# Kernel optimization log

Measured on AMD Instinct MI355X. Metric: run time of the kernel, lower is better.

Reference implementation:

```python
import jax, jax.numpy as jnp
import numpy as np
from jax import lax

B, H, W = 128, 128, 128
CHANS = [3, 32, 64, 128]   # convolution_structure
F, FH, FW = 128, 16, 16    # n_features, feature map size after 3 maxpools
P = FH * FW                # flatten_feature_size = 256
E, OUT = 32, 53            # expert_output_len, output_len


def _conv(x, w, b):
    # NCHW conv, 3x3, SAME padding, stride 1
    y = lax.conv_general_dilated(x, w, (1, 1), 'SAME',
                                 dimension_numbers=('NCHW', 'OIHW', 'NCHW'))
    return y + b[None, :, None, None]


def _maxpool2(x):
    return lax.reduce_window(x, -jnp.inf, lax.max,
                             (1, 1, 2, 2), (1, 1, 2, 2), 'VALID')


def setup_inputs() -> dict:
    key = jax.random.key(0)
    ks = jax.random.split(key, 16)

    def n(k, shape, fan_in):
        return jax.random.normal(k, shape, jnp.float32) / np.float32(np.sqrt(fan_in))

    inp = {'x': jax.random.normal(ks[0], (B, CHANS[0], H, W), jnp.float32)}
    for i in range(3):
        cin, cout = CHANS[i], CHANS[i + 1]
        inp[f'cw{i + 1}'] = n(ks[1 + i], (cout, cin, 3, 3), cin * 9)
        inp[f'cb{i + 1}'] = jnp.zeros((cout,), jnp.float32)
    inp['Wa'] = n(ks[4], (F, P), P)
    inp['ba'] = jnp.zeros((F,), jnp.float32)
    # per-expert MLP 256 -> 256 -> 128 -> 32 (128 experts, batched)
    inp['ew1'] = n(ks[5], (F, 256, 256), 256)
    inp['eb1'] = jnp.zeros((F, 256), jnp.float32)
    inp['ew2'] = n(ks[6], (F, 256, 128), 256)
    inp['eb2'] = jnp.zeros((F, 128), jnp.float32)
    inp['ew3'] = n(ks[7], (F, 128, E), 128)
    inp['eb3'] = jnp.zeros((F, E), jnp.float32)
    inp['fw'] = n(ks[8], (F * E, OUT), F * E)
    inp['fb'] = jnp.zeros((OUT,), jnp.float32)
    return inp


def reference(x, cw1, cb1, cw2, cb2, cw3, cb3, Wa, ba,
              ew1, eb1, ew2, eb2, ew3, eb3, fw, fb):
    # CNNBlock: (conv3x3 + ReLU + maxpool2) x 3  -> [B, F, 16, 16]
    h = x
    for w, b in ((cw1, cb1), (cw2, cb2), (cw3, cb3)):
        h = _maxpool2(jax.nn.relu(_conv(h, w, b)))
    feat = h.reshape(h.shape[0], F, P)                        # [B, F, 256]

    # AttentionBlock: per-feature scalar gate (attention_value = 1)
    att = jax.nn.sigmoid(jnp.einsum('bfp,fp->bf', feat, Wa) + ba)[:, :, None]

    # Experts: 128 independent gated MLPs, batched as grouped GEMMs
    z = feat * att                                            # input gating
    z = jax.nn.relu(jnp.einsum('bfp,fpq->bfq', z, ew1) + eb1)
    z = jax.nn.relu(jnp.einsum('bfp,fpq->bfq', z, ew2) + eb2)
    z = jnp.einsum('bfp,fpq->bfq', z, ew3) + eb3              # [B, F, 32]

    # outer ReLU over stacked expert outputs, flatten, final dense (att=1)
    z = jax.nn.relu(z).reshape(z.shape[0], -1)                # [B, 4096]
    return z @ fw + fb                                        # [B, 53]
```

## Files before the change

### kernel.cpp

```cpp
#include <hip/hip_runtime.h>
#include <hip/hip_bf16.h>
#include <math.h>

#define NF 128
#define NP 256

typedef __attribute__((ext_vector_type(8))) short bf16x8;
typedef __attribute__((ext_vector_type(4))) short bf16x4;
typedef __attribute__((ext_vector_type(4))) float f32x4;

#define GLOBAL_AS __attribute__((address_space(1)))
#define LDS_AS __attribute__((address_space(3)))

__global__ void __launch_bounds__(256) wpack_k(const float* __restrict__ w,
                                               __hip_bfloat16* __restrict__ wp,
                                               int COUT, int CIN)
{
    int i = blockIdx.x * 256 + threadIdx.x;
    int total = 9 * COUT * CIN;
    if (i >= total) return;
    int o  = i / (COUT * CIN);
    int r  = i - o * (COUT * CIN);
    int co = r / CIN, ci = r - co * CIN;
    wp[i] = __float2bfloat16(w[(size_t)(co * CIN + ci) * 9 + o]);
}

__global__ void __launch_bounds__(256) wpack1_k(const float* __restrict__ w,
                                                __hip_bfloat16* __restrict__ wp1)
{
    int i = blockIdx.x * 256 + threadIdx.x;
    if (i >= 2048) return;
    int s = i >> 10, co = (i >> 5) & 31, k = i & 31;
    int o = s * 8 + (k >> 2), ch = k & 3;
    float v = 0.f;
    if (o < 9 && ch < 3) v = w[(size_t)(co * 3 + ch) * 9 + o];
    wp1[i] = __float2bfloat16(v);
}

__global__ void __launch_bounds__(256) x2cl_k(const float* __restrict__ x,
                                              __hip_bfloat16* __restrict__ xb)
{
    int i = blockIdx.x * 256 + threadIdx.x;
    int b = i >> 14, rem = i & 16383;
    size_t base = ((size_t)b * 3) << 14;
    float v0 = x[base + rem];
    float v1 = x[base + 16384 + rem];
    float v2 = x[base + 32768 + rem];
    unsigned short hv[4];
    __hip_bfloat16 h0 = __float2bfloat16(v0);
    __hip_bfloat16 h1 = __float2bfloat16(v1);
    __hip_bfloat16 h2 = __float2bfloat16(v2);
    __builtin_memcpy(&hv[0], &h0, 2);
    __builtin_memcpy(&hv[1], &h1, 2);
    __builtin_memcpy(&hv[2], &h2, 2);
    hv[3] = 0;
    *(int2*)(xb + (size_t)i * 4) = *(const int2*)hv;
}

__global__ void __launch_bounds__(256) tpack_k(const float* __restrict__ in,
                                               __hip_bfloat16* __restrict__ out,
                                               int P, int Q, int qtiles)
{
    const int f  = blockIdx.y;
    const int pt = blockIdx.x / qtiles, qt = blockIdx.x - pt * qtiles;
    __shared__ float t[32][33];
    const float* src = in + (size_t)f * P * Q;
    __hip_bfloat16* dst = out + (size_t)f * P * Q;
    const int rr = threadIdx.x >> 5, c = threadIdx.x & 31;
    #pragma unroll
    for (int i = 0; i < 4; ++i)
        t[rr + i * 8][c] = src[(size_t)(pt * 32 + rr + i * 8) * Q + qt * 32 + c];
    __syncthreads();
    #pragma unroll
    for (int i = 0; i < 4; ++i)
        dst[(size_t)(qt * 32 + rr + i * 8) * P + pt * 32 + c] =
            __float2bfloat16(t[c][rr + i * 8]);
}

__global__ void __launch_bounds__(256) fwt_k(const float* __restrict__ fw, float* __restrict__ fwt)
{
    int i = blockIdx.x * 256 + threadIdx.x;
    if (i >= 53 * 4096) return;
    int o = i >> 12, k = i & 4095;
    fwt[i] = fw[(size_t)k * 53 + o];
}

__global__ void __launch_bounds__(256, 2) conv1_mfma(
    const __hip_bfloat16* __restrict__ xb,
    const __hip_bfloat16* __restrict__ wp1,
    const float* __restrict__ bias,
    __hip_bfloat16* __restrict__ out)
{
    __shared__ char lds[14 * 130 * 8];
    const int rb  = blockIdx.x * 8;
    const int b   = blockIdx.z;
    const int tid = threadIdx.x;

    #pragma unroll
    for (int t = 0; t < 8; ++t) {
        int u = tid + t * 256;
        if (u < 14 * 130) {
            int px = u % 130, row = u / 130;
            int gy = rb + row - 1, gx = px - 1;
            int2 v = make_int2(0, 0);
            if (gy >= 0 && gy < 128 && gx >= 0 && gx < 128)
                v = *(const int2*)(xb + (((size_t)b * 128 + gy) * 128 + gx) * 4);
            *(int2*)(lds + u * 8) = v;
        }
    }
    __syncthreads();

    const int w = tid >> 6, lane = tid & 63, p = lane & 15, q = lane >> 4;

    f32x4 acc[16][2];
    #pragma unroll
    for (int m = 0; m < 16; ++m)
        #pragma unroll
        for (int n = 0; n < 2; ++n) {
            acc[m][n][0] = 0.f; acc[m][n][1] = 0.f;
            acc[m][n][2] = 0.f; acc[m][n][3] = 0.f;
        }

    #pragma unroll
    for (int s = 0; s < 2; ++s) {
        bf16x8 bfr[2];
        #pragma unroll
        for (int n = 0; n < 2; ++n)
            bfr[n] = *(const bf16x8*)(wp1 + (size_t)(s * 32 + n * 16 + p) * 32 + q * 8);
        const int o0 = s * 8 + q * 2, o1 = o0 + 1;
        const int dy0 = o0 / 3, dx0 = o0 - 3 * dy0;
        const int dy1 = o1 / 3, dx1 = o1 - 3 * dy1;
        #pragma unroll
        for (int m = 0; m < 16; ++m) {
            const int mr = m >> 3, mx = m & 7;
            const int r0 = (2 * w + mr + dy0) * 130 + mx * 16 + p + dx0;
            const int r1 = (2 * w + mr + dy1) * 130 + mx * 16 + p + dx1;
            bf16x4 lo = *(const bf16x4*)(lds + r0 * 8);
            bf16x4 hi = *(const bf16x4*)(lds + r1 * 8);
            bf16x8 afr = __builtin_shufflevector(lo, hi, 0, 1, 2, 3, 4, 5, 6, 7);
            #pragma unroll
            for (int n = 0; n < 2; ++n)
                acc[m][n] = __builtin_amdgcn_mfma_f32_16x16x32_bf16(afr, bfr[n], acc[m][n], 0, 0, 0);
        }
    }

    const int prow = (rb >> 1) + w;
    float bv[2] = { bias[p], bias[16 + p] };
    #pragma unroll
    for (int mx = 0; mx < 8; ++mx)
        #pragma unroll
        for (int n = 0; n < 2; ++n) {
            f32x4 lo = acc[mx][n], hi = acc[8 + mx][n];
            float v0 = fmaxf(fmaxf(fmaxf(lo[0], lo[1]), fmaxf(hi[0], hi[1])) + bv[n], 0.f);
            float v1 = fmaxf(fmaxf(fmaxf(lo[2], lo[3]), fmaxf(hi[2], hi[3])) + bv[n], 0.f);
            int px = mx * 8 + q * 2;
            size_t base = ((size_t)(b * 64 + prow) * 64 + px) * 32 + n * 16 + p;
            out[base]      = __float2bfloat16(v0);
            out[base + 32] = __float2bfloat16(v1);
        }
}

template<int W, int CIN, int COUT, int SWZ, int OUTF>
__global__ void __launch_bounds__(256, 2) conv_mfma(
    const __hip_bfloat16* __restrict__ in,
    const __hip_bfloat16* __restrict__ wp,
    const float* __restrict__ bias,
    __hip_bfloat16* __restrict__ outb,
    float* __restrict__ outf)
{
    constexpr int XW  = W / 16;
    constexpr int AF  = 2 * XW;
    constexpr int BF  = COUT / 16;
    constexpr int CH  = CIN / 8;
    constexpr int KH  = CIN / 32;
    constexpr int PXW = W + 2;
    constexpr int UNITS  = 10 * PXW * CH;
    constexpr int NIT    = (UNITS + 255) / 256;
    constexpr int STAGEB = UNITS * 16;
    constexpr int OUTLDS = OUTF ? (COUT * 68 * 4) : 0;
    constexpr int LDSB   = STAGEB > OUTLDS ? STAGEB : OUTLDS;

    __shared__ int4 ldsv[(LDSB + 15) / 16];
    char* ldsc = (char*)ldsv;

    const int rb  = blockIdx.x * 8;
    const int b   = blockIdx.z;
    const int tid = threadIdx.x;

    #pragma unroll
    for (int t = 0; t < NIT; ++t) {
        int u = tid + t * 256;
        if (u < UNITS) {
            int ch = u % CH; int pl = u / CH;
            int xx = pl % PXW; int row = pl / PXW;
            int gy = rb + row - 1, gx = xx - 1;
            if (gy >= 0 && gy < W && gx >= 0 && gx < W) {
                int ch_src = SWZ ? (ch ^ (pl & 7)) : ch;
                const __hip_bfloat16* gp = in + ((size_t)(b * W + gy) * W + gx) * CIN + ch_src * 8;
                char* lb = ldsc + (size_t)(t * 256 + (tid & ~63)) * 16;
                __builtin_amdgcn_global_load_lds(
                    (const GLOBAL_AS void*)gp, (LDS_AS void*)lb, 16, 0, 0);
            } else {
                *(int4*)(ldsc + (size_t)u * 16) = make_int4(0, 0, 0, 0);
            }
        }
    }
    __syncthreads();

    const int w = tid >> 6, lane = tid & 63, p = lane & 15, q = lane >> 4;

    f32x4 acc[AF][BF];
    #pragma unroll
    for (int m = 0; m < AF; ++m)
        #pragma unroll
        for (int n = 0; n < BF; ++n) {
            acc[m][n][0] = 0.f; acc[m][n][1] = 0.f;
            acc[m][n][2] = 0.f; acc[m][n][3] = 0.f;
        }

    float bv[BF];
    #pragma unroll
    for (int n = 0; n < BF; ++n) bv[n] = bias[n * 16 + p];

    #pragma unroll 1
    for (int o = 0; o < 9; ++o) {
        const int ky = o / 3, kx = o - 3 * (o / 3);
        #pragma unroll
        for (int h = 0; h < KH; ++h) {
            bf16x8 bfr[BF];
            #pragma unroll
            for (int n = 0; n < BF; ++n)
                bfr[n] = *(const bf16x8*)(wp + (size_t)(o * COUT + n * 16 + p) * CIN + h * 32 + q * 8);
            bf16x8 afr[AF];
            #pragma unroll
            for (int m = 0; m < AF; ++m) {
                const int mr = m / XW, mx = m % XW;
                const int pix = (2 * w + mr + ky) * PXW + mx * 16 + kx + p;
                const int ch = h * 4 + q;
                const int slot = SWZ ? (pix * CH + (ch ^ (pix & 7))) : (pix * CH + ch);
                afr[m] = *(const bf16x8*)(ldsc + slot * 16);
            }
            #pragma unroll
            for (int m = 0; m < AF; ++m)
                #pragma unroll
                for (int n = 0; n < BF; ++n)
                    acc[m][n] = __builtin_amdgcn_mfma_f32_16x16x32_bf16(afr[m], bfr[n], acc[m][n], 0, 0, 0);
        }
    }

    const int prow = (rb >> 1) + w;
    if constexpr (OUTF == 0) {
        #pragma unroll
        for (int mx = 0; mx < XW; ++mx)
            #pragma unroll
            for (int n = 0; n < BF; ++n) {
                f32x4 lo = acc[mx][n], hi = acc[XW + mx][n];
                float v0 = fmaxf(fmaxf(fmaxf(lo[0], lo[1]), fmaxf(hi[0], hi[1])) + bv[n], 0.f);
                float v1 = fmaxf(fmaxf(fmaxf(lo[2], lo[3]), fmaxf(hi[2], hi[3])) + bv[n], 0.f);
                int px = mx * 8 + q * 2;
                size_t base = ((size_t)(b * (W / 2) + prow) * (W / 2) + px) * COUT + n * 16 + p;
                outb[base]        = __float2bfloat16(v0);
                outb[base + COUT] = __float2bfloat16(v1);
            }
    } else {
        __syncthreads();
        float* fl = (float*)ldsc;
        #pragma unroll
        for (int mx = 0; mx < XW; ++mx)
            #pragma unroll
            for (int n = 0; n < BF; ++n) {
                f32x4 lo = acc[mx][n], hi = acc[XW + mx][n];
                float v0 = fmaxf(fmaxf(fmaxf(lo[0], lo[1]), fmaxf(hi[0], hi[1])) + bv[n], 0.f);
                float v1 = fmaxf(fmaxf(fmaxf(lo[2], lo[3]), fmaxf(hi[2], hi[3])) + bv[n], 0.f);
                int px = mx * 8 + q * 2;
                fl[(n * 16 + p) * 68 + w * 16 + px]     = v0;
                fl[(n * 16 + p) * 68 + w * 16 + px + 1] = v1;
            }
        __syncthreads();
        for (int i = tid; i < COUT * 16; i += 256) {
            int c = i >> 4, j4 = i & 15;
            float4 vv = *(const float4*)&fl[c * 68 + j4 * 4];
            *(float4*)(outf + (size_t)(b * COUT + c) * 256 + (rb >> 1) * 16 + j4 * 4) = vv;
        }
    }
}

__global__ void __launch_bounds__(256) attention_k(
    const float* __restrict__ feat, const float* __restrict__ Wa,
    const float* __restrict__ ba, float* __restrict__ att)
{
    const int wid  = blockIdx.x * 4 + (threadIdx.x >> 6);
    const int lane = threadIdx.x & 63;
    const int b = wid >> 7, f = wid & 127;

    const float4 a  = ((const float4*)&feat[((size_t)b * NF + f) * NP])[lane];
    const float4 wv = ((const float4*)&Wa[(size_t)f * NP])[lane];
    float s = a.x * wv.x + a.y * wv.y + a.z * wv.z + a.w * wv.w;
    #pragma unroll
    for (int off = 32; off; off >>= 1) s += __shfl_down(s, off);
    if (lane == 0) att[b * NF + f] = 1.f / (1.f + expf(-(s + ba[f])));
}

__global__ void __launch_bounds__(256, 2) experts_mfma(
    const float* __restrict__ feat, const float* __restrict__ att,
    const __hip_bfloat16* __restrict__ w1, const float* __restrict__ eb1,
    const __hip_bfloat16* __restrict__ w2, const float* __restrict__ eb2,
    const __hip_bfloat16* __restrict__ w3, const float* __restrict__ eb3,
    float* __restrict__ z)
{
    const int f  = blockIdx.x;
    const int r0 = blockIdx.y * 32;
    const int tid = threadIdx.x;

    __shared__ char lds[32768];
    char* Xb  = lds;
    char* H1b = lds + 16384;
    char* H2b = lds;

    for (int u = tid; u < 32 * 32; u += 256) {
        int row = u >> 5, ch = u & 31;
        int b = r0 + row;
        const float* src = feat + ((size_t)b * NF + f) * NP + ch * 8;
        float g = att[b * NF + f];
        float4 v0 = *(const float4*)src;
        float4 v1 = *(const float4*)(src + 4);
        unsigned short hv[8];
        float vv[8] = {v0.x, v0.y, v0.z, v0.w, v1.x, v1.y, v1.z, v1.w};
        #pragma unroll
        for (int j = 0; j < 8; ++j) {
            __hip_bfloat16 hb = __float2bfloat16(vv[j] * g);
            __builtin_memcpy(&hv[j], &hb, 2);
        }
        int slot = row * 32 + (ch ^ (row & 7));
        *(int4*)(Xb + slot * 16) = *(const int4*)hv;
    }
    __syncthreads();

    const int wv = tid >> 6, lane = tid & 63, p = lane & 15, q = lane >> 4;
    const int rh = wv & 1, cf = wv >> 1;
    const int mrow = rh * 16;

    f32x4 acc1[8];
    #pragma unroll
    for (int n = 0; n < 8; ++n) { acc1[n][0]=0.f; acc1[n][1]=0.f; acc1[n][2]=0.f; acc1[n][3]=0.f; }
    #pragma unroll
    for (int k = 0; k < 8; ++k) {
        bf16x8 bfr[8];
        #pragma unroll
        for (int n = 0; n < 8; ++n)
            bfr[n] = *(const bf16x8*)(w1 + ((size_t)f * 256 + cf * 128 + n * 16 + p) * 256 + k * 32 + q * 8);
        int row = mrow + p, ch = k * 4 + q;
        bf16x8 afr = *(const bf16x8*)(Xb + (row * 32 + (ch ^ (row & 7))) * 16);
        #pragma unroll
        for (int n = 0; n < 8; ++n)
            acc1[n] = __builtin_amdgcn_mfma_f32_16x16x32_bf16(afr, bfr[n], acc1[n], 0, 0, 0);
    }
    #pragma unroll
    for (int n = 0; n < 8; ++n) {
        int col = cf * 128 + n * 16 + p;
        float bb = eb1[(size_t)f * 256 + col];
        #pragma unroll
        for (int reg = 0; reg < 4; ++reg) {
            float v = fmaxf(acc1[n][reg] + bb, 0.f);
            int row = mrow + q * 4 + reg;
            int slot = row * 32 + ((col >> 3) ^ (row & 7));
            *(__hip_bfloat16*)(H1b + slot * 16 + (col & 7) * 2) = __float2bfloat16(v);
        }
    }
    __syncthreads();

    f32x4 acc2[4];
    #pragma unroll
    for (int n = 0; n < 4; ++n) { acc2[n][0]=0.f; acc2[n][1]=0.f; acc2[n][2]=0.f; acc2[n][3]=0.f; }
    #pragma unroll
    for (int k = 0; k < 8; ++k) {
        bf16x8 bfr[4];
        #pragma unroll
        for (int n = 0; n < 4; ++n)
            bfr[n] = *(const bf16x8*)(w2 + ((size_t)f * 128 + cf * 64 + n * 16 + p) * 256 + k * 32 + q * 8);
        int row = mrow + p, ch = k * 4 + q;
        bf16x8 afr = *(const bf16x8*)(H1b + (row * 32 + (ch ^ (row & 7))) * 16);
        #pragma unroll
        for (int n = 0; n < 4; ++n)
            acc2[n] = __builtin_amdgcn_mfma_f32_16x16x32_bf16(afr, bfr[n], acc2[n], 0, 0, 0);
    }
    #pragma unroll
    for (int n = 0; n < 4; ++n) {
        int col = cf * 64 + n * 16 + p;
        float bb = eb2[(size_t)f * 128 + col];
        #pragma unroll
        for (int reg = 0; reg < 4; ++reg) {
            float v = fmaxf(acc2[n][reg] + bb, 0.f);
            int row = mrow + q * 4 + reg;
            int slot = row * 16 + ((col >> 3) ^ (row & 7));
            *(__hip_bfloat16*)(H2b + slot * 16 + (col & 7) * 2) = __float2bfloat16(v);
        }
    }
    __syncthreads();

    f32x4 acc3;
    acc3[0]=0.f; acc3[1]=0.f; acc3[2]=0.f; acc3[3]=0.f;
    #pragma unroll
    for (int k = 0; k < 4; ++k) {
        bf16x8 bfr = *(const bf16x8*)(w3 + ((size_t)f * 32 + cf * 16 + p) * 128 + k * 32 + q * 8);
        int row = mrow + p, ch = k * 4 + q;
        bf16x8 afr = *(const bf16x8*)(H2b + (row * 16 + (ch ^ (row & 7))) * 16);
        acc3 = __builtin_amdgcn_mfma_f32_16x16x32_bf16(afr, bfr, acc3, 0, 0, 0);
    }
    {
        float bb = eb3[(size_t)f * 32 + cf * 16 + p];
        #pragma unroll
        for (int reg = 0; reg < 4; ++reg) {
            float v = fmaxf(acc3[reg] + bb, 0.f);
            int row = r0 + mrow + q * 4 + reg;
            z[(size_t)row * 4096 + f * 32 + cf * 16 + p] = v;
        }
    }
}

__global__ void __launch_bounds__(256) final_k(
    const float* __restrict__ z, const float* __restrict__ fwt,
    const float* __restrict__ fb, float* __restrict__ out)
{
    const int b  = blockIdx.x;
    const int og = blockIdx.y;
    __shared__ float zs[4096];
    for (int i = threadIdx.x; i < 1024; i += 256)
        *(float4*)&zs[i * 4] = *(const float4*)&z[(size_t)b * 4096 + i * 4];
    __syncthreads();

    const int wv = threadIdx.x >> 6, lane = threadIdx.x & 63;
    const int o = og * 4 + wv;
    if (o >= 53) return;
    const float4* wr = (const float4*)&fwt[(size_t)o * 4096];
    float s = 0.f;
    #pragma unroll
    for (int it = 0; it < 16; ++it) {
        float4 zv = *(const float4*)&zs[(it * 64 + lane) * 4];
        float4 w4 = wr[it * 64 + lane];
        s += zv.x * w4.x + zv.y * w4.y + zv.z * w4.z + zv.w * w4.w;
    }
    #pragma unroll
    for (int off = 32; off; off >>= 1) s += __shfl_down(s, off);
    if (lane == 0) out[b * 53 + o] = s + fb[o];
}

extern "C" void kernel_launch(void* const* d_in, const int* in_sizes, int n_in,
                              void* d_out, int out_size, void* d_ws, size_t ws_size,
                              hipStream_t stream)
{
    const float* x   = (const float*)d_in[0];
    const float* cw1 = (const float*)d_in[1];
    const float* cb1 = (const float*)d_in[2];
    const float* cw2 = (const float*)d_in[3];
    const float* cb2 = (const float*)d_in[4];
    const float* cw3 = (const float*)d_in[5];
    const float* cb3 = (const float*)d_in[6];
    const float* Wa  = (const float*)d_in[7];
    const float* ba  = (const float*)d_in[8];
    const float* ew1 = (const float*)d_in[9];
    const float* eb1 = (const float*)d_in[10];
    const float* ew2 = (const float*)d_in[11];
    const float* eb2 = (const float*)d_in[12];
    const float* ew3 = (const float*)d_in[13];
    const float* eb3 = (const float*)d_in[14];
    const float* fw  = (const float*)d_in[15];
    const float* fb  = (const float*)d_in[16];

    float* ws = (float*)d_ws;
    __hip_bfloat16* p1b  = (__hip_bfloat16*)ws;
    __hip_bfloat16* p2b  = (__hip_bfloat16*)(ws + 8388608);
    float* feat = ws + 12582912;
    float* att  = ws + 16777216;
    __hip_bfloat16* wp2  = (__hip_bfloat16*)(ws + 16793600);
    __hip_bfloat16* wp3  = (__hip_bfloat16*)(ws + 16802816);
    __hip_bfloat16* ew1b = (__hip_bfloat16*)(ws + 16839680);
    __hip_bfloat16* ew2b = (__hip_bfloat16*)(ws + 21033984);
    __hip_bfloat16* ew3b = (__hip_bfloat16*)(ws + 23131136);
    float* fwt = ws + 23393280;
    __hip_bfloat16* wp1b = (__hip_bfloat16*)(ws + 23610368);
    __hip_bfloat16* xb   = (__hip_bfloat16*)(ws + 23611392);
    float* z   = ws;

    wpack1_k<<<8, 256, 0, stream>>>(cw1, wp1b);
    wpack_k<<<72, 256, 0, stream>>>(cw2, wp2, 64, 32);
    wpack_k<<<288, 256, 0, stream>>>(cw3, wp3, 128, 64);
    tpack_k<<<dim3(64, 128), 256, 0, stream>>>(ew1, ew1b, 256, 256, 8);
    tpack_k<<<dim3(32, 128), 256, 0, stream>>>(ew2, ew2b, 256, 128, 4);
    tpack_k<<<dim3(4, 128), 256, 0, stream>>>(ew3, ew3b, 128, 32, 1);
    fwt_k<<<848, 256, 0, stream>>>(fw, fwt);

    x2cl_k<<<8192, 256, 0, stream>>>(x, xb);
    conv1_mfma<<<dim3(16, 1, 128), 256, 0, stream>>>(xb, wp1b, cb1, p1b);
    conv_mfma<64, 32, 64, 0, 0><<<dim3(8, 1, 128), 256, 0, stream>>>(p1b, wp2, cb2, p2b, nullptr);
    conv_mfma<32, 64, 128, 1, 1><<<dim3(4, 1, 128), 256, 0, stream>>>(p2b, wp3, cb3, nullptr, feat);
    attention_k<<<4096, 256, 0, stream>>>(feat, Wa, ba, att);
    experts_mfma<<<dim3(128, 4), 256, 0, stream>>>(feat, att, ew1b, eb1, ew2b, eb2, ew3b, eb3, z);
    final_k<<<dim3(128, 14), 256, 0, stream>>>(z, fwt, fb, (float*)d_out);
}
```

Before: 168.8 us.

## Fuse input conversion into conv1 and prefetch conv weight fragments

Removes the separate fp32-to-bf16 channels-last conversion kernel and has conv1 read the NCHW fp32 input directly, converting while it stages into LDS. This drops one launch and a round trip of the converted input through memory, at the cost of three strided scalar loads per pixel inside conv1. Separately, the conv_mfma main loop is flattened over (tap, k-half) steps and the next step's weight fragments are loaded while the current step's MFMAs run. The first weights are also issued before the LDS barrier, to hide global load latency at the cost of extra registers.

```diff
diff --git a/kernel.cpp b/kernel.cpp
--- a/kernel.cpp
+++ b/kernel.cpp
@@ -37,26 +37,6 @@
     wp1[i] = __float2bfloat16(v);
 }
 
-__global__ void __launch_bounds__(256) x2cl_k(const float* __restrict__ x,
-                                              __hip_bfloat16* __restrict__ xb)
-{
-    int i = blockIdx.x * 256 + threadIdx.x;
-    int b = i >> 14, rem = i & 16383;
-    size_t base = ((size_t)b * 3) << 14;
-    float v0 = x[base + rem];
-    float v1 = x[base + 16384 + rem];
-    float v2 = x[base + 32768 + rem];
-    unsigned short hv[4];
-    __hip_bfloat16 h0 = __float2bfloat16(v0);
-    __hip_bfloat16 h1 = __float2bfloat16(v1);
-    __hip_bfloat16 h2 = __float2bfloat16(v2);
-    __builtin_memcpy(&hv[0], &h0, 2);
-    __builtin_memcpy(&hv[1], &h1, 2);
-    __builtin_memcpy(&hv[2], &h2, 2);
-    hv[3] = 0;
-    *(int2*)(xb + (size_t)i * 4) = *(const int2*)hv;
-}
-
 __global__ void __launch_bounds__(256) tpack_k(const float* __restrict__ in,
                                                __hip_bfloat16* __restrict__ out,
                                                int P, int Q, int qtiles)
@@ -86,7 +66,7 @@
 }
 
 __global__ void __launch_bounds__(256, 2) conv1_mfma(
-    const __hip_bfloat16* __restrict__ xb,
+    const float* __restrict__ x,
     const __hip_bfloat16* __restrict__ wp1,
     const float* __restrict__ bias,
     __hip_bfloat16* __restrict__ out)
@@ -102,10 +82,17 @@
         if (u < 14 * 130) {
             int px = u % 130, row = u / 130;
             int gy = rb + row - 1, gx = px - 1;
-            int2 v = make_int2(0, 0);
-            if (gy >= 0 && gy < 128 && gx >= 0 && gx < 128)
-                v = *(const int2*)(xb + (((size_t)b * 128 + gy) * 128 + gx) * 4);
-            *(int2*)(lds + u * 8) = v;
+            unsigned short hv[4] = {0, 0, 0, 0};
+            if (gy >= 0 && gy < 128 && gx >= 0 && gx < 128) {
+                size_t base = (((size_t)b * 3) * 128 + gy) * 128 + gx;
+                __hip_bfloat16 h0 = __float2bfloat16(x[base]);
+                __hip_bfloat16 h1 = __float2bfloat16(x[base + 16384]);
+                __hip_bfloat16 h2 = __float2bfloat16(x[base + 32768]);
+                __builtin_memcpy(&hv[0], &h0, 2);
+                __builtin_memcpy(&hv[1], &h1, 2);
+                __builtin_memcpy(&hv[2], &h2, 2);
+            }
+            *(int2*)(lds + u * 8) = *(const int2*)hv;
         }
     }
     __syncthreads();
@@ -173,6 +160,7 @@
     constexpr int BF  = COUT / 16;
     constexpr int CH  = CIN / 8;
     constexpr int KH  = CIN / 32;
+    constexpr int NSTEP = 9 * KH;
     constexpr int PXW = W + 2;
     constexpr int UNITS  = 10 * PXW * CH;
     constexpr int NIT    = (UNITS + 255) / 256;
@@ -186,6 +174,7 @@
     const int rb  = blockIdx.x * 8;
     const int b   = blockIdx.z;
     const int tid = threadIdx.x;
+    const int w = tid >> 6, lane = tid & 63, p = lane & 15, q = lane >> 4;
 
     #pragma unroll
     for (int t = 0; t < NIT; ++t) {
@@ -205,9 +194,13 @@
             }
         }
     }
-    __syncthreads();
-
-    const int w = tid >> 6, lane = tid & 63, p = lane & 15, q = lane >> 4;
+
+    bf16x8 bcur[BF], bnxt[BF];
+    #pragma unroll
+    for (int n = 0; n < BF; ++n)
+        bcur[n] = *(const bf16x8*)(wp + (size_t)(n * 16 + p) * CIN + q * 8);
+
+    __syncthreads();
 
     f32x4 acc[AF][BF];
     #pragma unroll
@@ -223,29 +216,36 @@
     for (int n = 0; n < BF; ++n) bv[n] = bias[n * 16 + p];
 
     #pragma unroll 1
-    for (int o = 0; o < 9; ++o) {
+    for (int s = 0; s < NSTEP; ++s) {
+        const int o  = (KH == 1) ? s : (s >> 1);
+        const int h  = (KH == 1) ? 0 : (s & 1);
         const int ky = o / 3, kx = o - 3 * (o / 3);
-        #pragma unroll
-        for (int h = 0; h < KH; ++h) {
-            bf16x8 bfr[BF];
+
+        if (s + 1 < NSTEP) {
+            const int o2 = (KH == 1) ? (s + 1) : ((s + 1) >> 1);
+            const int h2 = (KH == 1) ? 0 : ((s + 1) & 1);
             #pragma unroll
             for (int n = 0; n < BF; ++n)
-                bfr[n] = *(const bf16x8*)(wp + (size_t)(o * COUT + n * 16 + p) * CIN + h * 32 + q * 8);
-            bf16x8 afr[AF];
+                bnxt[n] = *(const bf16x8*)(wp + (size_t)(o2 * COUT + n * 16 + p) * CIN + h2 * 32 + q * 8);
+        }
+
+        bf16x8 afr[AF];
+        #pragma unroll
+        for (int m = 0; m < AF; ++m) {
+            const int mr = m / XW, mx = m % XW;
+            const int pix = (2 * w + mr + ky) * PXW + mx * 16 + kx + p;
+            const int ch = h * 4 + q;
+            const int slot = SWZ ? (pix * CH + (ch ^ (pix & 7))) : (pix * CH + ch);
+            afr[m] = *(const bf16x8*)(ldsc + slot * 16);
+        }
+        #pragma unroll
+        for (int m = 0; m < AF; ++m)
             #pragma unroll
-            for (int m = 0; m < AF; ++m) {
-                const int mr = m / XW, mx = m % XW;
-                const int pix = (2 * w + mr + ky) * PXW + mx * 16 + kx + p;
-                const int ch = h * 4 + q;
-                const int slot = SWZ ? (pix * CH + (ch ^ (pix & 7))) : (pix * CH + ch);
-                afr[m] = *(const bf16x8*)(ldsc + slot * 16);
-            }
-            #pragma unroll
-            for (int m = 0; m < AF; ++m)
-                #pragma unroll
-                for (int n = 0; n < BF; ++n)
-                    acc[m][n] = __builtin_amdgcn_mfma_f32_16x16x32_bf16(afr[m], bfr[n], acc[m][n], 0, 0, 0);
-        }
+            for (int n = 0; n < BF; ++n)
+                acc[m][n] = __builtin_amdgcn_mfma_f32_16x16x32_bf16(afr[m], bcur[n], acc[m][n], 0, 0, 0);
+
+        #pragma unroll
+        for (int n = 0; n < BF; ++n) bcur[n] = bnxt[n];
     }
 
     const int prow = (rb >> 1) + w;
@@ -479,7 +479,6 @@
     __hip_bfloat16* ew3b = (__hip_bfloat16*)(ws + 23131136);
     float* fwt = ws + 23393280;
     __hip_bfloat16* wp1b = (__hip_bfloat16*)(ws + 23610368);
-    __hip_bfloat16* xb   = (__hip_bfloat16*)(ws + 23611392);
     float* z   = ws;
 
     wpack1_k<<<8, 256, 0, stream>>>(cw1, wp1b);
@@ -490,8 +489,7 @@
     tpack_k<<<dim3(4, 128), 256, 0, stream>>>(ew3, ew3b, 128, 32, 1);
     fwt_k<<<848, 256, 0, stream>>>(fw, fwt);
 
-    x2cl_k<<<8192, 256, 0, stream>>>(x, xb);
-    conv1_mfma<<<dim3(16, 1, 128), 256, 0, stream>>>(xb, wp1b, cb1, p1b);
+    conv1_mfma<<<dim3(16, 1, 128), 256, 0, stream>>>(x, wp1b, cb1, p1b);
     conv_mfma<64, 32, 64, 0, 0><<<dim3(8, 1, 128), 256, 0, stream>>>(p1b, wp2, cb2, p2b, nullptr);
     conv_mfma<32, 64, 128, 1, 1><<<dim3(4, 1, 128), 256, 0, stream>>>(p2b, wp3, cb3, nullptr, feat);
     attention_k<<<4096, 256, 0, stream>>>(feat, Wa, ba, att);
```

New measurement: 161.1 us. 1.05x faster.
